# Kernel optimization log

Measured on AMD Instinct MI355X. Metric: run time of the kernel, lower is better.

The kernel has to match this reference:

```python
import jax, jax.numpy as jnp
import numpy as np

EMB = 128
HID = 128
N = 1024


def setup_inputs() -> dict:
    key = jax.random.key(0)
    ks = jax.random.split(key, 10)
    s1 = 1.0 / np.sqrt(2 * EMB)
    s2 = 1.0 / np.sqrt(HID)
    return {
        "z1": jax.random.normal(ks[0], (N, EMB), jnp.float32),
        "z2": jax.random.normal(ks[1], (N, EMB), jnp.float32),
        "W1": jax.random.uniform(ks[2], (HID, 2 * EMB), jnp.float32, -s1, s1),
        "b1": jax.random.uniform(ks[3], (HID,), jnp.float32, -s1, s1),
        "W2": jax.random.uniform(ks[4], (HID, HID), jnp.float32, -s2, s2),
        "b2": jax.random.uniform(ks[5], (HID,), jnp.float32, -s2, s2),
        "W3": jax.random.uniform(ks[6], (1, HID), jnp.float32, -s2, s2),
        "b3": jax.random.uniform(ks[7], (1,), jnp.float32, -s2, s2),
    }


def reference(z1, z2, W1, b1, W2, b2, W3, b3):
    # pairs[i, j] = concat(z1[j], z2[i]); first Linear split into two matmuls
    # so the [n, n, 2*emb] concat tensor is never materialized (same math).
    W1a = W1[:, :EMB]   # acts on z1 half
    W1b = W1[:, EMB:]   # acts on z2 half
    a = jnp.einsum('jd,hd->jh', z1, W1a)          # [n, h], varies along j
    b = jnp.einsum('id,hd->ih', z2, W1b)          # [n, h], varies along i
    h1 = jax.nn.gelu(a[None, :, :] + b[:, None, :] + b1, approximate=False)  # [n, n, h]
    h2 = jax.nn.gelu(jnp.einsum('ijh,gh->ijg', h1, W2) + b2, approximate=False)
    log_q = jnp.einsum('ijh,oh->ijo', h2, W3) + b3  # [n, n, 1]
    return log_q[..., 0]
```

## Files before the change

kernel.cpp:

```cpp
#include <hip/hip_runtime.h>

#define NN  1024
#define EMB 128
#define HID 128

typedef __attribute__((ext_vector_type(4))) float float4v;
typedef __attribute__((ext_vector_type(8))) float float8v;
typedef __attribute__((ext_vector_type(8))) short short8;
typedef __attribute__((ext_vector_type(4))) __bf16 bf16x4;
typedef __attribute__((ext_vector_type(8))) __bf16 bf16x8;

__device__ __forceinline__ short8 to_bf16x8(float4v a, float4v b) {
  float8v f = {a[0], a[1], a[2], a[3], b[0], b[1], b[2], b[3]};
  bf16x8 r = __builtin_convertvector(f, bf16x8);
  return __builtin_bit_cast(short8, r);
}

__device__ __forceinline__ void store_bf16x4(short* p, float4v v) {
  bf16x4 r = __builtin_convertvector(v, bf16x4);
  *(bf16x4*)p = r;
}

__device__ __forceinline__ float4v gelu4(float4v x) {
  float4v x2 = x * x;
  float4v t = x2 * 0.1029432f + 2.3022086f;
  float4v y = x * t;
  float4v e;
  e[0] = __builtin_amdgcn_exp2f(y[0]);
  e[1] = __builtin_amdgcn_exp2f(y[1]);
  e[2] = __builtin_amdgcn_exp2f(y[2]);
  e[3] = __builtin_amdgcn_exp2f(y[3]);
  float4v d = e + 1.0f;
  float p01 = d[0] * d[1];
  float p23 = d[2] * d[3];
  float rall = __builtin_amdgcn_rcpf(p01 * p23);
  float r01 = p23 * rall;
  float r23 = p01 * rall;
  float4v rv;
  rv[0] = d[1] * r01;
  rv[1] = d[0] * r01;
  rv[2] = d[3] * r23;
  rv[3] = d[2] * r23;
  return x - x * rv;
}

__device__ __forceinline__ float4v mfma16(short8 a, short8 b, float4v c) {
  return __builtin_amdgcn_mfma_f32_16x16x32_bf16(a, b, c, 0, 0, 0);
}

__global__ __launch_bounds__(256)
void prep_kernel(const float* __restrict__ z1, const float* __restrict__ z2,
                 const float* __restrict__ W1, const float* __restrict__ b1,
                 const float* __restrict__ W2,
                 float* __restrict__ Abuf, float* __restrict__ Bbuf,
                 unsigned short* __restrict__ W2f) {
  int blk = blockIdx.x, tid = threadIdx.x;
  if (blk < 256) {
    int which = blk >> 7;
    int j0 = ((blk & 127) >> 1) << 4;
    int hh = blk & 1;
    const float* z = which ? z2 : z1;
    __shared__ __align__(16) short zf[4 * 64 * 8];
    __shared__ __align__(16) short w1f[16 * 64 * 8];

#pragma unroll
    for (int p = 0; p < 2; ++p) {
      int u = p * 256 + tid;
      int row = u >> 5;
      int c = (u & 31) * 4;
      float4v v = *(const float4v*)(z + (j0 + row) * EMB + c);
      int kt = c >> 5;
      int lane = ((c >> 3) & 3) * 16 + row;
      store_bf16x4(zf + (kt * 64 + lane) * 8 + (c & 7), v);
    }
    {
      const float* wbase = W1 + (hh * 64) * (2 * EMB) + which * EMB;
#pragma unroll
      for (int p = 0; p < 8; ++p) {
        int u = p * 256 + tid;
        int grow = u >> 5;
        int c = (u & 31) * 4;
        float4v v = *(const float4v*)(wbase + grow * (2 * EMB) + c);
        int kt = c >> 5;
        int ntl = grow >> 4;
        int lane = ((c >> 3) & 3) * 16 + (grow & 15);
        store_bf16x4(w1f + ((kt * 4 + ntl) * 64 + lane) * 8 + (c & 7), v);
      }
    }
    __syncthreads();

    int w = tid >> 6, l = tid & 63, r = l & 15, q = l >> 4;
    float4v acc = {};
#pragma unroll
    for (int kt = 0; kt < 4; ++kt) {
      short8 az = *(const short8*)(zf + (kt * 64 + l) * 8);
      short8 bf = *(const short8*)(w1f + ((kt * 4 + w) * 64 + l) * 8);
      acc = mfma16(az, bf, acc);
    }
    int gg = hh * 64 + w * 16 + r;
    float ba = which ? 0.0f : b1[gg];
    float* dstp = which ? Bbuf : Abuf;
#pragma unroll
    for (int reg = 0; reg < 4; ++reg)
      dstp[(j0 + q * 4 + reg) * HID + gg] = acc[reg] + ba;
  } else {
    int s0 = (blk - 256) * 2048 + tid * 8;
    float4v v0 = *(const float4v*)(W2 + s0);
    float4v v1 = *(const float4v*)(W2 + s0 + 4);
    float vals[8] = {v0[0], v0[1], v0[2], v0[3], v1[0], v1[1], v1[2], v1[3]};
#pragma unroll
    for (int j = 0; j < 8; ++j) {
      int s = s0 + j;
      int g = s >> 7;
      int h = s & 127;
      int kt = h >> 5;
      int nt = g >> 4;
      int lane = ((h >> 3) & 3) * 16 + (g & 15);
      int dst = ((kt * 8 + nt) * 64 + lane) * 8 + (h & 7);
      unsigned u = __float_as_uint(vals[j]);
      W2f[dst] = (unsigned short)((u + 0x7FFFu + ((u >> 16) & 1u)) >> 16);
    }
  }
}

__global__ __launch_bounds__(256, 4)
void fused_mlp_kernel(const float* __restrict__ Abuf, const float* __restrict__ Bbuf,
                      const float* __restrict__ W2f4,
                      const float* __restrict__ b2, const float* __restrict__ W3,
                      const float* __restrict__ b3, float* __restrict__ out) {
  __shared__ __align__(16) short s_w2[HID * HID];

  int tid = threadIdx.x;
  {
    const float4v* src = (const float4v*)W2f4;
    float4v* dst = (float4v*)s_w2;
#pragma unroll
    for (int t = 0; t < 8; ++t)
      dst[tid + t * 256] = src[tid + t * 256];
  }

  int w = tid >> 6, l = tid & 63, r = l & 15, q = l >> 4;
  int bi = (blockIdx.x >> 6) << 3;
  int bj = (blockIdx.x & 63) << 4;

  const float* Arow = Abuf + (bj + r) * HID;
  const float* B0 = Bbuf + (bi + 2 * w) * HID;
  const float* B1 = B0 + HID;

  float4v acc[2][8];
#pragma unroll
  for (int nt = 0; nt < 8; ++nt) {
    float4v bv = *(const float4v*)(b2 + nt * 16 + q * 4);
    acc[0][nt] = bv;
    acc[1][nt] = bv;
  }

  __syncthreads();

#pragma unroll
  for (int kt = 0; kt < 4; ++kt) {
    int h0 = kt * 32 + q * 8;
    float4v a0 = *(const float4v*)(Arow + h0);
    float4v a1 = *(const float4v*)(Arow + h0 + 4);

    short8 af0 = to_bf16x8(gelu4(a0 + *(const float4v*)(B0 + h0)),
                           gelu4(a1 + *(const float4v*)(B0 + h0 + 4)));
    short8 af1 = to_bf16x8(gelu4(a0 + *(const float4v*)(B1 + h0)),
                           gelu4(a1 + *(const float4v*)(B1 + h0 + 4)));

    const short8* wrow = (const short8*)s_w2 + kt * 8 * 64 + l;
#pragma unroll
    for (int nt = 0; nt < 8; ++nt) {
      short8 wf = wrow[nt * 64];
      acc[0][nt] = mfma16(wf, af0, acc[0][nt]);
      acc[1][nt] = mfma16(wf, af1, acc[1][nt]);
    }
  }

  float bias3 = b3[0];
#pragma unroll
  for (int p = 0; p < 2; ++p) {
    float4v s = {0.f, 0.f, 0.f, 0.f};
#pragma unroll
    for (int nt = 0; nt < 8; ++nt) {
      float4v wv = *(const float4v*)(W3 + nt * 16 + q * 4);
      s = s + gelu4(acc[p][nt]) * wv;
    }
    float sc = s[0] + s[1] + s[2] + s[3];
    sc += __shfl_xor(sc, 16, 64);
    sc += __shfl_xor(sc, 32, 64);
    if (l < 16)
      out[(bi + 2 * w + p) * NN + bj + l] = sc + bias3;
  }
}

extern "C" void kernel_launch(void* const* d_in, const int* in_sizes, int n_in,
                              void* d_out, int out_size, void* d_ws, size_t ws_size,
                              hipStream_t stream) {
  const float* z1 = (const float*)d_in[0];
  const float* z2 = (const float*)d_in[1];
  const float* W1 = (const float*)d_in[2];
  const float* b1 = (const float*)d_in[3];
  const float* W2 = (const float*)d_in[4];
  const float* b2 = (const float*)d_in[5];
  const float* W3 = (const float*)d_in[6];
  const float* b3 = (const float*)d_in[7];
  float* out = (float*)d_out;

  float* Abuf = (float*)d_ws;
  float* Bbuf = Abuf + NN * HID;
  unsigned short* W2f = (unsigned short*)(Bbuf + NN * HID);

  prep_kernel<<<264, 256, 0, stream>>>(z1, z2, W1, b1, W2, Abuf, Bbuf, W2f);
  fused_mlp_kernel<<<(NN / 8) * (NN / 16), 256, 0, stream>>>(
      Abuf, Bbuf, (const float*)W2f, b2, W3, b3, out);
}
```

Before: 158.1 us.

## Split second-layer output columns into two halves and prefetch A/B loads

The second matmul now runs in two passes over output column halves, so only 8 accumulator vectors are live instead of 16. The GELU'd bf16 activation fragments are cached in registers and reused in the second pass. The A/B inputs for the next k-step are prefetched before the current step's GELU work. The aim is lower register pressure, so the kernel can reach its launch-bounds occupancy target, plus hiding global load latency. In exchange, the afs array keeps 8 short8 values live and the epilogue is split into two stages.

Result: no change. 157.3 us (-0.5%).

```diff
diff --git a/kernel.cpp b/kernel.cpp
--- a/kernel.cpp
+++ b/kernel.cpp
@@ -143,54 +143,99 @@
   int bi = (blockIdx.x >> 6) << 3;
   int bj = (blockIdx.x & 63) << 4;
 
-  const float* Arow = Abuf + (bj + r) * HID;
-  const float* B0 = Bbuf + (bi + 2 * w) * HID;
-  const float* B1 = B0 + HID;
-
-  float4v acc[2][8];
-#pragma unroll
-  for (int nt = 0; nt < 8; ++nt) {
+  const float* Ap  = Abuf + (bj + r) * HID + q * 8;
+  const float* Bp0 = Bbuf + (bi + 2 * w) * HID + q * 8;
+  const float* Bp1 = Bp0 + HID;
+
+  short8 afs[4][2];
+  float4v s0 = {0.f, 0.f, 0.f, 0.f};
+  float4v s1 = {0.f, 0.f, 0.f, 0.f};
+  float4v acc[2][4];
+
+  __syncthreads();
+
+#pragma unroll
+  for (int nt = 0; nt < 4; ++nt) {
     float4v bv = *(const float4v*)(b2 + nt * 16 + q * 4);
     acc[0][nt] = bv;
     acc[1][nt] = bv;
   }
 
-  __syncthreads();
+  float4v a0  = *(const float4v*)(Ap);
+  float4v a1  = *(const float4v*)(Ap + 4);
+  float4v b00 = *(const float4v*)(Bp0);
+  float4v b01 = *(const float4v*)(Bp0 + 4);
+  float4v b10 = *(const float4v*)(Bp1);
+  float4v b11 = *(const float4v*)(Bp1 + 4);
 
 #pragma unroll
   for (int kt = 0; kt < 4; ++kt) {
-    int h0 = kt * 32 + q * 8;
-    float4v a0 = *(const float4v*)(Arow + h0);
-    float4v a1 = *(const float4v*)(Arow + h0 + 4);
-
-    short8 af0 = to_bf16x8(gelu4(a0 + *(const float4v*)(B0 + h0)),
-                           gelu4(a1 + *(const float4v*)(B0 + h0 + 4)));
-    short8 af1 = to_bf16x8(gelu4(a0 + *(const float4v*)(B1 + h0)),
-                           gelu4(a1 + *(const float4v*)(B1 + h0 + 4)));
-
-    const short8* wrow = (const short8*)s_w2 + kt * 8 * 64 + l;
-#pragma unroll
-    for (int nt = 0; nt < 8; ++nt) {
+    float4v ca0 = a0, ca1 = a1, cb00 = b00, cb01 = b01, cb10 = b10, cb11 = b11;
+    if (kt < 3) {
+      int off = (kt + 1) * 32;
+      a0  = *(const float4v*)(Ap + off);
+      a1  = *(const float4v*)(Ap + off + 4);
+      b00 = *(const float4v*)(Bp0 + off);
+      b01 = *(const float4v*)(Bp0 + off + 4);
+      b10 = *(const float4v*)(Bp1 + off);
+      b11 = *(const float4v*)(Bp1 + off + 4);
+    }
+    short8 af0 = to_bf16x8(gelu4(ca0 + cb00), gelu4(ca1 + cb01));
+    short8 af1 = to_bf16x8(gelu4(ca0 + cb10), gelu4(ca1 + cb11));
+    afs[kt][0] = af0;
+    afs[kt][1] = af1;
+
+    const short8* wrow = (const short8*)s_w2 + kt * 512 + l;
+#pragma unroll
+    for (int nt = 0; nt < 4; ++nt) {
       short8 wf = wrow[nt * 64];
       acc[0][nt] = mfma16(wf, af0, acc[0][nt]);
       acc[1][nt] = mfma16(wf, af1, acc[1][nt]);
     }
   }
 
+#pragma unroll
+  for (int nt = 0; nt < 4; ++nt) {
+    float4v wv = *(const float4v*)(W3 + nt * 16 + q * 4);
+    s0 = s0 + gelu4(acc[0][nt]) * wv;
+    s1 = s1 + gelu4(acc[1][nt]) * wv;
+  }
+
+#pragma unroll
+  for (int nt = 0; nt < 4; ++nt) {
+    float4v bv = *(const float4v*)(b2 + (nt + 4) * 16 + q * 4);
+    acc[0][nt] = bv;
+    acc[1][nt] = bv;
+  }
+#pragma unroll
+  for (int kt = 0; kt < 4; ++kt) {
+    short8 af0 = afs[kt][0];
+    short8 af1 = afs[kt][1];
+    const short8* wrow = (const short8*)s_w2 + kt * 512 + 4 * 64 + l;
+#pragma unroll
+    for (int nt = 0; nt < 4; ++nt) {
+      short8 wf = wrow[nt * 64];
+      acc[0][nt] = mfma16(wf, af0, acc[0][nt]);
+      acc[1][nt] = mfma16(wf, af1, acc[1][nt]);
+    }
+  }
+#pragma unroll
+  for (int nt = 0; nt < 4; ++nt) {
+    float4v wv = *(const float4v*)(W3 + (nt + 4) * 16 + q * 4);
+    s0 = s0 + gelu4(acc[0][nt]) * wv;
+    s1 = s1 + gelu4(acc[1][nt]) * wv;
+  }
+
   float bias3 = b3[0];
-#pragma unroll
-  for (int p = 0; p < 2; ++p) {
-    float4v s = {0.f, 0.f, 0.f, 0.f};
-#pragma unroll
-    for (int nt = 0; nt < 8; ++nt) {
-      float4v wv = *(const float4v*)(W3 + nt * 16 + q * 4);
-      s = s + gelu4(acc[p][nt]) * wv;
-    }
-    float sc = s[0] + s[1] + s[2] + s[3];
-    sc += __shfl_xor(sc, 16, 64);
-    sc += __shfl_xor(sc, 32, 64);
-    if (l < 16)
-      out[(bi + 2 * w + p) * NN + bj + l] = sc + bias3;
+  float sc0 = s0[0] + s0[1] + s0[2] + s0[3];
+  float sc1 = s1[0] + s1[1] + s1[2] + s1[3];
+  sc0 += __shfl_xor(sc0, 16, 64);
+  sc0 += __shfl_xor(sc0, 32, 64);
+  sc1 += __shfl_xor(sc1, 16, 64);
+  sc1 += __shfl_xor(sc1, 32, 64);
+  if (l < 16) {
+    out[(bi + 2 * w) * NN + bj + l]     = sc0 + bias3;
+    out[(bi + 2 * w + 1) * NN + bj + l] = sc1 + bias3;
   }
 }
 
```
